# Kernel optimization log

Hardware: AMD Instinct MI355X
Metric: run time of the kernel (lower is better)

Reference implementation:

```python
import jax, jax.numpy as jnp
import numpy as np

N_NODES = 50000
D_FEAT = 128
HIDDEN = 256
CLASSES = 40
N_EDGES = 800000


def setup_inputs() -> dict:
    key = jax.random.key(0)
    ks = jax.random.split(key, 8)
    x = jax.random.normal(ks[0], (N_NODES, D_FEAT), dtype=jnp.float32)
    edge_index = jax.random.randint(ks[1], (2, N_EDGES), 0, N_NODES, dtype=jnp.int64)
    s1 = 1.0 / np.sqrt(D_FEAT)
    s2 = 1.0 / np.sqrt(HIDDEN)
    # PyG SAGEConv: lin_l (applied to aggregated neighbors, has bias), lin_r (root, no bias)
    Wl1 = jax.random.uniform(ks[2], (HIDDEN, D_FEAT), jnp.float32, -s1, s1)
    bl1 = jnp.zeros((HIDDEN,), jnp.float32)
    Wr1 = jax.random.uniform(ks[3], (HIDDEN, D_FEAT), jnp.float32, -s1, s1)
    Wl2 = jax.random.uniform(ks[4], (CLASSES, HIDDEN), jnp.float32, -s2, s2)
    bl2 = jnp.zeros((CLASSES,), jnp.float32)
    Wr2 = jax.random.uniform(ks[5], (CLASSES, HIDDEN), jnp.float32, -s2, s2)
    return {"x": x, "edge_index": edge_index, "Wl1": Wl1, "bl1": bl1, "Wr1": Wr1,
            "Wl2": Wl2, "bl2": bl2, "Wr2": Wr2}


def _mean_aggregate(x, src, dst, n_nodes):
    # gather source features along edges, scatter-mean into destinations
    summed = jax.ops.segment_sum(x[src], dst, num_segments=n_nodes)  # [N, d]
    counts = jax.ops.segment_sum(jnp.ones((src.shape[0],), x.dtype), dst,
                                 num_segments=n_nodes)
    return summed / jnp.maximum(counts, 1.0)[:, None]


def _sage_conv(x, src, dst, Wl, bl, Wr):
    agg = _mean_aggregate(x, src, dst, x.shape[0])
    return agg @ Wl.T + bl + x @ Wr.T


def reference(x, edge_index, Wl1, bl1, Wr1, Wl2, bl2, Wr2):
    src, dst = edge_index[0], edge_index[1]
    h = _sage_conv(x, src, dst, Wl1, bl1, Wr1)
    h = jax.nn.relu(h)
    # F.dropout(training=self.training): eval-mode inference -> identity
    h = _sage_conv(h, src, dst, Wl2, bl2, Wr2)
    return jax.nn.log_softmax(h, axis=1)
```

## Files before the change

### kernel.cpp

```cpp
#include <hip/hip_runtime.h>
#include <hip/hip_bf16.h>
#include <math.h>

#define N_NODES 50000
#define D_FEAT  128
#define HIDDEN  256
#define CLASSES 40
#define N_EDGES 800000
#define P2S 64
#define R2S 48
#define SCAN_NB 196
#define HLS 264
#define NTILES 3125
#define GRID_L 512
#define NBUCK 196
#define BCAP  5120

typedef unsigned int  u32;
typedef unsigned short u16;
typedef __attribute__((ext_vector_type(8))) short short8;
typedef __attribute__((ext_vector_type(4))) float floatx4;

__device__ __forceinline__ float bf_lo(u32 w) { union { u32 i; float f; } u; u.i = w << 16; return u.f; }
__device__ __forceinline__ float bf_hi(u32 w) { union { u32 i; float f; } u; u.i = w & 0xffff0000u; return u.f; }
__device__ __forceinline__ float bf1(u16 h)   { union { u32 i; float f; } u; u.i = ((u32)h) << 16; return u.f; }
__device__ __forceinline__ u16 f2bf(float f) {
  union { float f; u32 i; } u; u.f = f; u32 i = u.i;
  return (u16)((i + 0x7fffu + ((i >> 16) & 1u)) >> 16);
}
__device__ __forceinline__ u32 packbf(float a, float b) { return (u32)f2bf(a) | ((u32)f2bf(b) << 16); }

__device__ __forceinline__ bool edges_are_i64(const void* eraw) {
  const long long* p = (const long long*)eraw;
  bool ok = true;
  #pragma unroll
  for (int i = 0; i < 8; i++) {
    long long v = p[(size_t)i * 100003];
    ok = ok && (v >= 0) && (v < N_NODES);
  }
  return ok;
}

__global__ __launch_bounds__(256) void bucketA_kernel(
    const void* __restrict__ eraw, int* __restrict__ bcur, u32* __restrict__ bbuf) {
  __shared__ int hist[NBUCK], base[NBUCK], loc[NBUCK];
  const bool i64f = edges_are_i64(eraw);
  const int t = threadIdx.x;
  for (int i = t; i < NBUCK; i += 256) { hist[i] = 0; loc[i] = 0; }
  __syncthreads();

  int sreg[16], dreg[16];
  const int e0 = blockIdx.x * 4096;
  #pragma unroll
  for (int j = 0; j < 16; j++) {
    int e = e0 + j * 256 + t;
    int ss = 0, dd = -1;
    if (e < N_EDGES) {
      if (i64f) {
        const long long* p = (const long long*)eraw;
        ss = (int)p[e]; dd = (int)p[N_EDGES + e];
      } else {
        const int* p = (const int*)eraw;
        ss = p[e]; dd = p[N_EDGES + e];
      }
      if ((u32)ss >= N_NODES || (u32)dd >= N_NODES) dd = -1;
    }
    sreg[j] = ss; dreg[j] = dd;
    if (dd >= 0) atomicAdd(&hist[dd >> 8], 1);
  }
  __syncthreads();
  for (int i = t; i < NBUCK; i += 256)
    base[i] = atomicAdd(&bcur[i], hist[i]);
  __syncthreads();
  #pragma unroll
  for (int j = 0; j < 16; j++) {
    int dd = dreg[j];
    if (dd >= 0) {
      int bk = dd >> 8;
      int pos = base[bk] + atomicAdd(&loc[bk], 1);
      if (pos < BCAP)
        bbuf[(size_t)bk * BCAP + pos] = (u32)sreg[j] | ((u32)(dd & 255) << 16);
    }
  }
}

__global__ __launch_bounds__(256) void bscan_kernel(
    const u32* __restrict__ bbuf, const int* __restrict__ bcur,
    int* __restrict__ offsets, int* __restrict__ blocksums) {
  __shared__ int cnt[256];
  __shared__ int lds[256];
  const int t = threadIdx.x;
  const int b = blockIdx.x;
  cnt[t] = 0;
  __syncthreads();
  const int n = min(bcur[b], BCAP);
  for (int i = t; i < n; i += 256) {
    u32 e = bbuf[(size_t)b * BCAP + i];
    atomicAdd(&cnt[(e >> 16) & 255], 1);
  }
  __syncthreads();
  int c = cnt[t];
  lds[t] = c;
  __syncthreads();
  #pragma unroll
  for (int d = 1; d < 256; d <<= 1) {
    int v = (t >= d) ? lds[t - d] : 0;
    __syncthreads();
    lds[t] += v;
    __syncthreads();
  }
  offsets[b * 256 + t] = lds[t] - c;
  if (t == 255) blocksums[b] = lds[255];
}

__global__ __launch_bounds__(256) void scan2_kernel(
    const int* __restrict__ blocksums, int* __restrict__ btops,
    int* __restrict__ offsets) {
  __shared__ int lds[256];
  const int t = threadIdx.x;
  int c = (t < SCAN_NB) ? blocksums[t] : 0;
  lds[t] = c;
  __syncthreads();
  #pragma unroll
  for (int d = 1; d < 256; d <<= 1) {
    int v = (t >= d) ? lds[t - d] : 0;
    __syncthreads();
    lds[t] += v;
    __syncthreads();
  }
  if (t < SCAN_NB) btops[t] = lds[t] - c;
  if (t == SCAN_NB - 1) offsets[N_NODES] = lds[t];
}

__global__ __launch_bounds__(256) void bucketB_kernel(
    const u32* __restrict__ bbuf, const int* __restrict__ bcur,
    const int* __restrict__ btops, int* __restrict__ offsets,
    int* __restrict__ csr) {
  __shared__ int cur[256];
  const int t = threadIdx.x;
  const int b = blockIdx.x;
  const int node = b * 256 + t;
  int off = 0;
  if (node < N_NODES) {
    off = offsets[node] + btops[b];
    offsets[node] = off;
  }
  cur[t] = off;
  __syncthreads();
  const int n = min(bcur[b], BCAP);
  for (int i = t; i < n; i += 256) {
    u32 e = bbuf[(size_t)b * BCAP + i];
    int dl = (e >> 16) & 255;
    int pos = atomicAdd(&cur[dl], 1);
    csr[pos] = (int)(e & 0xFFFFu);
  }
}

__global__ __launch_bounds__(256) void cvt_all_kernel(
    const float* __restrict__ x,
    const float* __restrict__ Wl1, const float* __restrict__ Wr1,
    const float* __restrict__ Wl2, const float* __restrict__ Wr2,
    u16* __restrict__ xb, u16* __restrict__ wb) {
  if (blockIdx.x < 6250) {
    int i = (blockIdx.x * 256 + threadIdx.x) * 4;
    float4 v = *(const float4*)(x + i);
    u32* o = (u32*)(xb + i);
    o[0] = packbf(v.x, v.y);
    o[1] = packbf(v.z, v.w);
  } else {
    int i = (blockIdx.x - 6250) * 256 + threadIdx.x;
    if (i < 32768)      wb[i] = f2bf(Wl1[i]);
    else if (i < 65536) wb[i] = f2bf(Wr1[i - 32768]);
    else if (i < 75776) wb[i] = f2bf(Wl2[i - 65536]);
    else if (i < 86016) wb[i] = f2bf(Wr2[i - 75776]);
  }
}

__global__ __launch_bounds__(256) void gather1_kernel(
    const u16* __restrict__ xb, const int* __restrict__ offsets,
    const int* __restrict__ csr_src, u16* __restrict__ agg1) {
  const int node = blockIdx.x * 4 + (threadIdx.x >> 6);
  const int lane = threadIdx.x & 63;
  int b = offsets[node], e = offsets[node + 1];
  float a0 = 0.f, a1 = 0.f, b0 = 0.f, b1 = 0.f;
  float c0 = 0.f, c1 = 0.f, d0 = 0.f, d1 = 0.f;
  float e0 = 0.f, e1 = 0.f, f0 = 0.f, f1 = 0.f;
  float g0 = 0.f, g1 = 0.f, h0 = 0.f, h1 = 0.f;
  int i = b;
  for (; i + 8 <= e; i += 8) {
    int s0 = csr_src[i],     s1 = csr_src[i + 1], s2 = csr_src[i + 2], s3 = csr_src[i + 3];
    int s4 = csr_src[i + 4], s5 = csr_src[i + 5], s6 = csr_src[i + 6], s7 = csr_src[i + 7];
    u32 w0 = ((const u32*)(xb + (size_t)s0 * D_FEAT))[lane];
    u32 w1 = ((const u32*)(xb + (size_t)s1 * D_FEAT))[lane];
    u32 w2 = ((const u32*)(xb + (size_t)s2 * D_FEAT))[lane];
    u32 w3 = ((const u32*)(xb + (size_t)s3 * D_FEAT))[lane];
    u32 w4 = ((const u32*)(xb + (size_t)s4 * D_FEAT))[lane];
    u32 w5 = ((const u32*)(xb + (size_t)s5 * D_FEAT))[lane];
    u32 w6 = ((const u32*)(xb + (size_t)s6 * D_FEAT))[lane];
    u32 w7 = ((const u32*)(xb + (size_t)s7 * D_FEAT))[lane];
    a0 += bf_lo(w0); a1 += bf_hi(w0);
    b0 += bf_lo(w1); b1 += bf_hi(w1);
    c0 += bf_lo(w2); c1 += bf_hi(w2);
    d0 += bf_lo(w3); d1 += bf_hi(w3);
    e0 += bf_lo(w4); e1 += bf_hi(w4);
    f0 += bf_lo(w5); f1 += bf_hi(w5);
    g0 += bf_lo(w6); g1 += bf_hi(w6);
    h0 += bf_lo(w7); h1 += bf_hi(w7);
  }
  for (; i < e; i++) {
    int s = csr_src[i];
    u32 w = ((const u32*)(xb + (size_t)s * D_FEAT))[lane];
    a0 += bf_lo(w); a1 += bf_hi(w);
  }
  float s0 = ((a0 + b0) + (c0 + d0)) + ((e0 + f0) + (g0 + h0));
  float s1 = ((a1 + b1) + (c1 + d1)) + ((e1 + f1) + (g1 + h1));
  float inv = 1.0f / (float)max(e - b, 1);
  ((u32*)(agg1 + (size_t)node * D_FEAT))[lane] = packbf(s0 * inv, s1 * inv);
}

__global__ __launch_bounds__(256, 2) void layer_kernel(
    const u16* __restrict__ agg1, const u16* __restrict__ xb,
    const u16* __restrict__ Wl1b, const u16* __restrict__ Wr1b,
    const float* __restrict__ bl1,
    const u16* __restrict__ Wl2b, const u16* __restrict__ Wr2b,
    const float* __restrict__ bl2,
    u16* __restrict__ p2b, float* __restrict__ r2f) {
  __shared__ u16 h_lds[16 * HLS];
  const int lane = threadIdx.x & 63;
  const int wave = threadIdx.x >> 6;
  const int n15  = lane & 15;
  const int quad = lane >> 4;
  const int ko   = quad * 8;
  const int colbase = wave * 64;

  short8 Bf[8][4];
  #pragma unroll
  for (int s = 0; s < 8; s++) {
    const u16* W = (s < 4) ? Wl1b : Wr1b;
    const int kk = (s & 3) * 32;
    #pragma unroll
    for (int t = 0; t < 4; t++)
      Bf[s][t] = *(const short8*)(W + (size_t)(colbase + t * 16 + n15) * D_FEAT + ko + kk);
  }

  const int  c0   = wave;
  const bool isR0 = (c0 >= 3);
  const int  tc0  = c0 - (isR0 ? 3 : 0);
  const int  wr0  = min(tc0 * 16 + n15, CLASSES - 1);
  const u16* Wc0  = (isR0 ? Wr2b : Wl2b) + (size_t)wr0 * HIDDEN + ko;
  const bool has1 = (wave < 2);
  const int  tc1  = wave + 1;
  const int  wr1  = min(tc1 * 16 + n15, CLASSES - 1);
  const u16* Wc1  = Wr2b + (size_t)wr1 * HIDDEN + ko;

  const float bias0 = bl2[min(tc0 * 16 + n15, CLASSES - 1)];
  const float bias1 = bl2[min(tc1 * 16 + n15, CLASSES - 1)];

  for (int tile = blockIdx.x; tile < NTILES; tile += GRID_L) {
    const int m0 = tile * 16;
    {
      const u16* A0 = agg1 + (size_t)(m0 + n15) * D_FEAT + ko;
      const u16* A1 = xb   + (size_t)(m0 + n15) * D_FEAT + ko;

      floatx4 acc[4];
      #pragma unroll
      for (int t = 0; t < 4; t++) acc[t] = floatx4{0.f, 0.f, 0.f, 0.f};

      short8 a[4];
      #pragma unroll
      for (int s = 0; s < 4; s++) a[s] = *(const short8*)(A0 + s * 32);
      #pragma unroll
      for (int s = 0; s < 4; s++)
        #pragma unroll
        for (int t = 0; t < 4; t++)
          acc[t] = __builtin_amdgcn_mfma_f32_16x16x32_bf16(a[s], Bf[s][t], acc[t], 0, 0, 0);
      #pragma unroll
      for (int s = 0; s < 4; s++) a[s] = *(const short8*)(A1 + s * 32);
      #pragma unroll
      for (int s = 0; s < 4; s++)
        #pragma unroll
        for (int t = 0; t < 4; t++)
          acc[t] = __builtin_amdgcn_mfma_f32_16x16x32_bf16(a[s], Bf[4 + s][t], acc[t], 0, 0, 0);

      #pragma unroll
      for (int t = 0; t < 4; t++) {
        int col = colbase + t * 16 + n15;
        float bias = bl1[col];
        #pragma unroll
        for (int r = 0; r < 4; r++) {
          float v = acc[t][r] + bias;
          v = v > 0.f ? v : 0.f;
          h_lds[(quad * 4 + r) * HLS + col] = f2bf(v);
        }
      }
    }
    __syncthreads();
    {
      floatx4 acc0 = floatx4{0.f, 0.f, 0.f, 0.f};
      floatx4 acc1 = floatx4{0.f, 0.f, 0.f, 0.f};
      #pragma unroll
      for (int s = 0; s < 8; s++) {
        short8 a2 = *(const short8*)(&h_lds[n15 * HLS + s * 32 + ko]);
        acc0 = __builtin_amdgcn_mfma_f32_16x16x32_bf16(a2, *(const short8*)(Wc0 + s * 32), acc0, 0, 0, 0);
        if (has1)
          acc1 = __builtin_amdgcn_mfma_f32_16x16x32_bf16(a2, *(const short8*)(Wc1 + s * 32), acc1, 0, 0, 0);
      }
      {
        int col = tc0 * 16 + n15;
        #pragma unroll
        for (int r = 0; r < 4; r++) {
          int row = m0 + quad * 4 + r;
          if (isR0) r2f[(size_t)row * R2S + col] = acc0[r] + bias0;
          else      p2b[(size_t)row * P2S + col] = f2bf(acc0[r]);
        }
      }
      if (has1) {
        int col = tc1 * 16 + n15;
        #pragma unroll
        for (int r = 0; r < 4; r++) {
          int row = m0 + quad * 4 + r;
          r2f[(size_t)row * R2S + col] = acc1[r] + bias1;
        }
      }
    }
    __syncthreads();
  }
}

__global__ __launch_bounds__(256) void final_kernel(
    const u16* __restrict__ p2b, const float* __restrict__ r2f,
    const int* __restrict__ offsets, const int* __restrict__ csr_src,
    float* __restrict__ out) {
  const int node = blockIdx.x * 4 + (threadIdx.x >> 6);
  const int lane = threadIdx.x & 63;
  int b = offsets[node], e = offsets[node + 1];
  float s[16];
  #pragma unroll
  for (int j = 0; j < 16; j++) s[j] = 0.f;
  int i = b;
  for (; i + 16 <= e; i += 16) {
    int c[16];
    #pragma unroll
    for (int j = 0; j < 16; j++) c[j] = csr_src[i + j];
    #pragma unroll
    for (int j = 0; j < 16; j++) s[j] += bf1(p2b[(size_t)c[j] * P2S + lane]);
  }
  for (; i + 8 <= e; i += 8) {
    int c[8];
    #pragma unroll
    for (int j = 0; j < 8; j++) c[j] = csr_src[i + j];
    #pragma unroll
    for (int j = 0; j < 8; j++) s[j] += bf1(p2b[(size_t)c[j] * P2S + lane]);
  }
  for (; i < e; i++) {
    int sc = csr_src[i];
    s[0] += bf1(p2b[(size_t)sc * P2S + lane]);
  }
  float sum4[4];
  #pragma unroll
  for (int j = 0; j < 4; j++)
    sum4[j] = (s[j] + s[j + 4]) + (s[j + 8] + s[j + 12]);
  float ssum = (sum4[0] + sum4[1]) + (sum4[2] + sum4[3]);
  float inv = 1.0f / (float)max(e - b, 1);
  const bool act = (lane < CLASSES);
  float v = act ? (ssum * inv + r2f[(size_t)node * R2S + lane]) : -INFINITY;
  float mx = v;
  #pragma unroll
  for (int d = 1; d < 64; d <<= 1) mx = fmaxf(mx, __shfl_xor(mx, d, 64));
  float ex = act ? expf(v - mx) : 0.f;
  float sum = ex;
  #pragma unroll
  for (int d = 1; d < 64; d <<= 1) sum += __shfl_xor(sum, d, 64);
  float l = mx + logf(sum);
  if (act) out[(size_t)node * CLASSES + lane] = v - l;
}

extern "C" void kernel_launch(void* const* d_in, const int* in_sizes, int n_in,
                              void* d_out, int out_size, void* d_ws, size_t ws_size,
                              hipStream_t stream) {
  const float* x   = (const float*)d_in[0];
  const void*  ei  = d_in[1];
  const float* Wl1 = (const float*)d_in[2];
  const float* bl1 = (const float*)d_in[3];
  const float* Wr1 = (const float*)d_in[4];
  const float* Wl2 = (const float*)d_in[5];
  const float* bl2 = (const float*)d_in[6];
  const float* Wr2 = (const float*)d_in[7];

  char* ws = (char*)d_ws;
  size_t off = 0;
  int* csr       = (int*)(ws + off); off += (size_t)N_EDGES * 4;
  int* offsets   = (int*)(ws + off); off += 204800;
  int* blocksums = (int*)(ws + off); off += 1024;
  int* btops     = (int*)(ws + off); off += 1024;
  int* bcur      = (int*)(ws + off); off += 1024;
  u32* bbuf      = (u32*)(ws + off); off += (size_t)NBUCK * BCAP * 4;
  u16* wb        = (u16*)(ws + off); off += 172288;
  u16* xb        = (u16*)(ws + off); off += (size_t)N_NODES * D_FEAT * 2;
  u16* agg1      = (u16*)(ws + off); off += (size_t)N_NODES * D_FEAT * 2;
  u16* p2b       = (u16*)(ws + off); off += (size_t)N_NODES * P2S * 2;
  float* r2f     = (float*)(ws + off); off += (size_t)N_NODES * R2S * 4;

  u16* Wl1b = wb;
  u16* Wr1b = wb + 32768;
  u16* Wl2b = wb + 65536;
  u16* Wr2b = wb + 75776;

  hipMemsetAsync(bcur, 0, NBUCK * 4, stream);
  cvt_all_kernel<<<6250 + 336, 256, 0, stream>>>(x, Wl1, Wr1, Wl2, Wr2, xb, wb);
  bucketA_kernel<<<NBUCK, 256, 0, stream>>>(ei, bcur, bbuf);
  bscan_kernel<<<NBUCK, 256, 0, stream>>>(bbuf, bcur, offsets, blocksums);
  scan2_kernel<<<1, 256, 0, stream>>>(blocksums, btops, offsets);
  bucketB_kernel<<<NBUCK, 256, 0, stream>>>(bbuf, bcur, btops, offsets, csr);
  gather1_kernel<<<N_NODES / 4, 256, 0, stream>>>(xb, offsets, csr, agg1);
  layer_kernel<<<GRID_L, 256, 0, stream>>>(agg1, xb, Wl1b, Wr1b, bl1,
                                           Wl2b, Wr2b, bl2, p2b, r2f);
  final_kernel<<<N_NODES / 4, 256, 0, stream>>>(p2b, r2f, offsets, csr, (float*)d_out);
}
```

Baseline: 227.9 us.

## Fuse conversion and CSR build into one cooperative kernel; stage layer tiles in LDS

Merges the bf16 conversion, bucket scatter, per-bucket scan, global scan and CSR fill into a single cooperative kernel of 196 blocks separated by grid syncs. This removes the memset and five separate launches. The bf16 conversion now runs on only 196 blocks in a grid-stride loop, which may cut bandwidth for that stage. The layer kernel also stages each 16-row tile of agg1 and xb into LDS with coalesced loads before the MFMA operand reads, which adds a block barrier per tile.

After: 315.4 us. 38.4% more time.

```diff
diff --git a/kernel.cpp b/kernel.cpp
--- a/kernel.cpp
+++ b/kernel.cpp
@@ -1,5 +1,6 @@
 #include <hip/hip_runtime.h>
 #include <hip/hip_bf16.h>
+#include <hip/hip_cooperative_groups.h>
 #include <math.h>
 
 #define N_NODES 50000
@@ -9,12 +10,15 @@
 #define N_EDGES 800000
 #define P2S 64
 #define R2S 48
-#define SCAN_NB 196
 #define HLS 264
+#define ALS 136
 #define NTILES 3125
 #define GRID_L 512
 #define NBUCK 196
 #define BCAP  5120
+#define CVT_BLKS 6586
+
+namespace cg = cooperative_groups;
 
 typedef unsigned int  u32;
 typedef unsigned short u16;
@@ -41,138 +45,132 @@
   return ok;
 }
 
-__global__ __launch_bounds__(256) void bucketA_kernel(
-    const void* __restrict__ eraw, int* __restrict__ bcur, u32* __restrict__ bbuf) {
-  __shared__ int hist[NBUCK], base[NBUCK], loc[NBUCK];
-  const bool i64f = edges_are_i64(eraw);
-  const int t = threadIdx.x;
-  for (int i = t; i < NBUCK; i += 256) { hist[i] = 0; loc[i] = 0; }
-  __syncthreads();
-
-  int sreg[16], dreg[16];
-  const int e0 = blockIdx.x * 4096;
-  #pragma unroll
-  for (int j = 0; j < 16; j++) {
-    int e = e0 + j * 256 + t;
-    int ss = 0, dd = -1;
-    if (e < N_EDGES) {
-      if (i64f) {
-        const long long* p = (const long long*)eraw;
-        ss = (int)p[e]; dd = (int)p[N_EDGES + e];
-      } else {
-        const int* p = (const int*)eraw;
-        ss = p[e]; dd = p[N_EDGES + e];
-      }
-      if ((u32)ss >= N_NODES || (u32)dd >= N_NODES) dd = -1;
-    }
-    sreg[j] = ss; dreg[j] = dd;
-    if (dd >= 0) atomicAdd(&hist[dd >> 8], 1);
-  }
-  __syncthreads();
-  for (int i = t; i < NBUCK; i += 256)
-    base[i] = atomicAdd(&bcur[i], hist[i]);
-  __syncthreads();
-  #pragma unroll
-  for (int j = 0; j < 16; j++) {
-    int dd = dreg[j];
-    if (dd >= 0) {
-      int bk = dd >> 8;
-      int pos = base[bk] + atomicAdd(&loc[bk], 1);
-      if (pos < BCAP)
-        bbuf[(size_t)bk * BCAP + pos] = (u32)sreg[j] | ((u32)(dd & 255) << 16);
-    }
-  }
-}
-
-__global__ __launch_bounds__(256) void bscan_kernel(
-    const u32* __restrict__ bbuf, const int* __restrict__ bcur,
-    int* __restrict__ offsets, int* __restrict__ blocksums) {
-  __shared__ int cnt[256];
-  __shared__ int lds[256];
-  const int t = threadIdx.x;
-  const int b = blockIdx.x;
-  cnt[t] = 0;
-  __syncthreads();
-  const int n = min(bcur[b], BCAP);
-  for (int i = t; i < n; i += 256) {
-    u32 e = bbuf[(size_t)b * BCAP + i];
-    atomicAdd(&cnt[(e >> 16) & 255], 1);
-  }
-  __syncthreads();
-  int c = cnt[t];
-  lds[t] = c;
-  __syncthreads();
-  #pragma unroll
-  for (int d = 1; d < 256; d <<= 1) {
-    int v = (t >= d) ? lds[t - d] : 0;
-    __syncthreads();
-    lds[t] += v;
-    __syncthreads();
-  }
-  offsets[b * 256 + t] = lds[t] - c;
-  if (t == 255) blocksums[b] = lds[255];
-}
-
-__global__ __launch_bounds__(256) void scan2_kernel(
-    const int* __restrict__ blocksums, int* __restrict__ btops,
-    int* __restrict__ offsets) {
-  __shared__ int lds[256];
-  const int t = threadIdx.x;
-  int c = (t < SCAN_NB) ? blocksums[t] : 0;
-  lds[t] = c;
-  __syncthreads();
-  #pragma unroll
-  for (int d = 1; d < 256; d <<= 1) {
-    int v = (t >= d) ? lds[t - d] : 0;
-    __syncthreads();
-    lds[t] += v;
-    __syncthreads();
-  }
-  if (t < SCAN_NB) btops[t] = lds[t] - c;
-  if (t == SCAN_NB - 1) offsets[N_NODES] = lds[t];
-}
-
-__global__ __launch_bounds__(256) void bucketB_kernel(
-    const u32* __restrict__ bbuf, const int* __restrict__ bcur,
-    const int* __restrict__ btops, int* __restrict__ offsets,
-    int* __restrict__ csr) {
-  __shared__ int cur[256];
-  const int t = threadIdx.x;
-  const int b = blockIdx.x;
-  const int node = b * 256 + t;
-  int off = 0;
-  if (node < N_NODES) {
-    off = offsets[node] + btops[b];
-    offsets[node] = off;
-  }
-  cur[t] = off;
-  __syncthreads();
-  const int n = min(bcur[b], BCAP);
-  for (int i = t; i < n; i += 256) {
-    u32 e = bbuf[(size_t)b * BCAP + i];
-    int dl = (e >> 16) & 255;
-    int pos = atomicAdd(&cur[dl], 1);
-    csr[pos] = (int)(e & 0xFFFFu);
-  }
-}
-
-__global__ __launch_bounds__(256) void cvt_all_kernel(
+__global__ __launch_bounds__(256) void prep_kernel(
     const float* __restrict__ x,
     const float* __restrict__ Wl1, const float* __restrict__ Wr1,
     const float* __restrict__ Wl2, const float* __restrict__ Wr2,
-    u16* __restrict__ xb, u16* __restrict__ wb) {
-  if (blockIdx.x < 6250) {
-    int i = (blockIdx.x * 256 + threadIdx.x) * 4;
-    float4 v = *(const float4*)(x + i);
-    u32* o = (u32*)(xb + i);
-    o[0] = packbf(v.x, v.y);
-    o[1] = packbf(v.z, v.w);
-  } else {
-    int i = (blockIdx.x - 6250) * 256 + threadIdx.x;
-    if (i < 32768)      wb[i] = f2bf(Wl1[i]);
-    else if (i < 65536) wb[i] = f2bf(Wr1[i - 32768]);
-    else if (i < 75776) wb[i] = f2bf(Wl2[i - 65536]);
-    else if (i < 86016) wb[i] = f2bf(Wr2[i - 75776]);
+    u16* __restrict__ xb, u16* __restrict__ wb,
+    const void* __restrict__ eraw, int* __restrict__ bcur,
+    u32* __restrict__ bbuf, int* __restrict__ blocksums,
+    int* __restrict__ offsets, int* __restrict__ csr) {
+  cg::grid_group grid = cg::this_grid();
+  __shared__ int s0[256], s1[256], s2[256];
+  const int t = threadIdx.x;
+  const int b = blockIdx.x;
+
+  if (t == 0) bcur[b] = 0;
+  for (int blk = b; blk < CVT_BLKS; blk += NBUCK) {
+    if (blk < 6250) {
+      int i = (blk * 256 + t) * 4;
+      float4 v = *(const float4*)(x + i);
+      u32* o = (u32*)(xb + i);
+      o[0] = packbf(v.x, v.y);
+      o[1] = packbf(v.z, v.w);
+    } else {
+      int i = (blk - 6250) * 256 + t;
+      if (i < 32768)      wb[i] = f2bf(Wl1[i]);
+      else if (i < 65536) wb[i] = f2bf(Wr1[i - 32768]);
+      else if (i < 75776) wb[i] = f2bf(Wl2[i - 65536]);
+      else if (i < 86016) wb[i] = f2bf(Wr2[i - 75776]);
+    }
+  }
+  grid.sync();
+
+  {
+    int* hist = s0; int* base = s1; int* loc = s2;
+    const bool i64f = edges_are_i64(eraw);
+    for (int i = t; i < NBUCK; i += 256) { hist[i] = 0; loc[i] = 0; }
+    __syncthreads();
+    int sreg[16], dreg[16];
+    const int e0 = b * 4096;
+    #pragma unroll
+    for (int j = 0; j < 16; j++) {
+      int e = e0 + j * 256 + t;
+      int ss = 0, dd = -1;
+      if (e < N_EDGES) {
+        if (i64f) {
+          const long long* p = (const long long*)eraw;
+          ss = (int)p[e]; dd = (int)p[N_EDGES + e];
+        } else {
+          const int* p = (const int*)eraw;
+          ss = p[e]; dd = p[N_EDGES + e];
+        }
+        if ((u32)ss >= N_NODES || (u32)dd >= N_NODES) dd = -1;
+      }
+      sreg[j] = ss; dreg[j] = dd;
+      if (dd >= 0) atomicAdd(&hist[dd >> 8], 1);
+    }
+    __syncthreads();
+    for (int i = t; i < NBUCK; i += 256)
+      base[i] = atomicAdd(&bcur[i], hist[i]);
+    __syncthreads();
+    #pragma unroll
+    for (int j = 0; j < 16; j++) {
+      int dd = dreg[j];
+      if (dd >= 0) {
+        int bk = dd >> 8;
+        int pos = base[bk] + atomicAdd(&loc[bk], 1);
+        if (pos < BCAP)
+          bbuf[(size_t)bk * BCAP + pos] = (u32)sreg[j] | ((u32)(dd & 255) << 16);
+      }
+    }
+  }
+  grid.sync();
+
+  {
+    int* cnt = s0; int* lds = s1;
+    cnt[t] = 0;
+    __syncthreads();
+    const int n = min(bcur[b], BCAP);
+    for (int i = t; i < n; i += 256) {
+      u32 e = bbuf[(size_t)b * BCAP + i];
+      atomicAdd(&cnt[(e >> 16) & 255], 1);
+    }
+    __syncthreads();
+    int c = cnt[t];
+    lds[t] = c;
+    __syncthreads();
+    #pragma unroll
+    for (int d = 1; d < 256; d <<= 1) {
+      int v = (t >= d) ? lds[t - d] : 0;
+      __syncthreads();
+      lds[t] += v;
+      __syncthreads();
+    }
+    offsets[b * 256 + t] = lds[t] - c;
+    if (t == 255) blocksums[b] = lds[255];
+  }
+  grid.sync();
+
+  {
+    int* slds = s0; int* cur = s1;
+    int c = (t < NBUCK) ? blocksums[t] : 0;
+    slds[t] = c;
+    __syncthreads();
+    #pragma unroll
+    for (int d = 1; d < 256; d <<= 1) {
+      int v = (t >= d) ? slds[t - d] : 0;
+      __syncthreads();
+      slds[t] += v;
+      __syncthreads();
+    }
+    const int btop = (b > 0) ? slds[b - 1] : 0;
+    if (b == NBUCK - 1 && t == 0) offsets[N_NODES] = slds[NBUCK - 1];
+    const int node = b * 256 + t;
+    int off = 0;
+    if (node < N_NODES) {
+      off = offsets[node] + btop;
+      offsets[node] = off;
+    }
+    cur[t] = off;
+    __syncthreads();
+    const int n = min(bcur[b], BCAP);
+    for (int i = t; i < n; i += 256) {
+      u32 e = bbuf[(size_t)b * BCAP + i];
+      int dl = (e >> 16) & 255;
+      int pos = atomicAdd(&cur[dl], 1);
+      csr[pos] = (int)(e & 0xFFFFu);
+    }
   }
 }
 
@@ -226,12 +224,16 @@
     const float* __restrict__ bl2,
     u16* __restrict__ p2b, float* __restrict__ r2f) {
   __shared__ u16 h_lds[16 * HLS];
+  __shared__ u16 a_lds[16 * ALS];
+  __shared__ u16 x_lds[16 * ALS];
   const int lane = threadIdx.x & 63;
   const int wave = threadIdx.x >> 6;
   const int n15  = lane & 15;
   const int quad = lane >> 4;
   const int ko   = quad * 8;
   const int colbase = wave * 64;
+  const int srow = (wave << 2) + quad;
+  const int scol = n15 * 8;
 
   short8 Bf[8][4];
   #pragma unroll
@@ -259,23 +261,26 @@
   for (int tile = blockIdx.x; tile < NTILES; tile += GRID_L) {
     const int m0 = tile * 16;
     {
-      const u16* A0 = agg1 + (size_t)(m0 + n15) * D_FEAT + ko;
-      const u16* A1 = xb   + (size_t)(m0 + n15) * D_FEAT + ko;
-
+      const size_t g = (size_t)(m0 + srow) * D_FEAT + scol;
+      *(short8*)(a_lds + srow * ALS + scol) = *(const short8*)(agg1 + g);
+      *(short8*)(x_lds + srow * ALS + scol) = *(const short8*)(xb + g);
+    }
+    __syncthreads();
+    {
       floatx4 acc[4];
       #pragma unroll
       for (int t = 0; t < 4; t++) acc[t] = floatx4{0.f, 0.f, 0.f, 0.f};
 
       short8 a[4];
       #pragma unroll
-      for (int s = 0; s < 4; s++) a[s] = *(const short8*)(A0 + s * 32);
+      for (int s = 0; s < 4; s++) a[s] = *(const short8*)(a_lds + n15 * ALS + ko + s * 32);
       #pragma unroll
       for (int s = 0; s < 4; s++)
         #pragma unroll
         for (int t = 0; t < 4; t++)
           acc[t] = __builtin_amdgcn_mfma_f32_16x16x32_bf16(a[s], Bf[s][t], acc[t], 0, 0, 0);
       #pragma unroll
-      for (int s = 0; s < 4; s++) a[s] = *(const short8*)(A1 + s * 32);
+      for (int s = 0; s < 4; s++) a[s] = *(const short8*)(x_lds + n15 * ALS + ko + s * 32);
       #pragma unroll
       for (int s = 0; s < 4; s++)
         #pragma unroll
@@ -392,7 +397,6 @@
   int* csr       = (int*)(ws + off); off += (size_t)N_EDGES * 4;
   int* offsets   = (int*)(ws + off); off += 204800;
   int* blocksums = (int*)(ws + off); off += 1024;
-  int* btops     = (int*)(ws + off); off += 1024;
   int* bcur      = (int*)(ws + off); off += 1024;
   u32* bbuf      = (u32*)(ws + off); off += (size_t)NBUCK * BCAP * 4;
   u16* wb        = (u16*)(ws + off); off += 172288;
@@ -406,12 +410,10 @@
   u16* Wl2b = wb + 65536;
   u16* Wr2b = wb + 75776;
 
-  hipMemsetAsync(bcur, 0, NBUCK * 4, stream);
-  cvt_all_kernel<<<6250 + 336, 256, 0, stream>>>(x, Wl1, Wr1, Wl2, Wr2, xb, wb);
-  bucketA_kernel<<<NBUCK, 256, 0, stream>>>(ei, bcur, bbuf);
-  bscan_kernel<<<NBUCK, 256, 0, stream>>>(bbuf, bcur, offsets, blocksums);
-  scan2_kernel<<<1, 256, 0, stream>>>(blocksums, btops, offsets);
-  bucketB_kernel<<<NBUCK, 256, 0, stream>>>(bbuf, bcur, btops, offsets, csr);
+  void* args[] = { (void*)&x, (void*)&Wl1, (void*)&Wr1, (void*)&Wl2, (void*)&Wr2,
+                   (void*)&xb, (void*)&wb, (void*)&ei, (void*)&bcur, (void*)&bbuf,
+                   (void*)&blocksums, (void*)&offsets, (void*)&csr };
+  hipLaunchCooperativeKernel((void*)prep_kernel, dim3(NBUCK), dim3(256), args, 0, stream);
   gather1_kernel<<<N_NODES / 4, 256, 0, stream>>>(xb, offsets, csr, agg1);
   layer_kernel<<<GRID_L, 256, 0, stream>>>(agg1, xb, Wl1b, Wr1b, bl1,
                                            Wl2b, Wr2b, bl2, p2b, r2f);
```
